# Kernel tuning notes

Hardware: AMD Instinct MI355X
Metric: run time of the kernel (lower is better)

The kernel has to match this reference:

```python
import jax, jax.numpy as jnp
import numpy as np

S = (256, 256, 256)          # MRI volume shape
N = 50000                    # number of Gaussians
T = 16                       # fixed tile edge; covers max bbox width = 2*3*sigma_max*(S-1)+2 <= 15
SIG_MIN, SIG_MAX = 0.004, 0.008  # NN-distance-based sigma range (k_sigma=1)


def setup_inputs() -> dict:
    key = jax.random.key(0)
    k1, k2, k3 = jax.random.split(key, 3)
    centers = jax.random.uniform(k1, (N, 3), dtype=jnp.float32)
    sigmas = jax.random.uniform(k2, (N,), dtype=jnp.float32, minval=SIG_MIN, maxval=SIG_MAX)
    intensities = jax.random.uniform(k3, (N,), dtype=jnp.float32)
    return {"centers": centers, "sigmas": sigmas, "intensities": intensities}


def _splat(centers, sigmas, intensities):
    dt = centers.dtype
    scale = jnp.asarray([s - 1 for s in S], dtype=dt)            # (3,) == scale_factors
    shape_f = jnp.asarray(S, dtype=dt)                           # (3,)
    shape_i = jnp.asarray(S, dtype=jnp.int32)                    # (3,)

    center_vox = centers * scale                                 # (N,3) voxel-space centers
    cutoff = 3.0 * sigmas[:, None] * scale                       # (N,3)
    # original: min_idx = max(c-cut, 0).int(); max_idx = (min(c+cut, scale)+1).int(), clipped to S
    min_idx = jnp.floor(jnp.maximum(center_vox - cutoff, 0.0)).astype(jnp.int32)          # (N,3)
    max_idx = jnp.minimum(jnp.floor(jnp.minimum(center_vox + cutoff, scale)) + 1.0,
                          shape_f).astype(jnp.int32)             # (N,3), exclusive

    ar = jnp.arange(T, dtype=jnp.int32)
    idx = min_idx[:, :, None] + ar[None, None, :]                # (N,3,T) absolute voxel idx
    valid = idx < max_idx[:, :, None]                            # (N,3,T) inside variable bbox
    idx_c = jnp.minimum(idx, shape_i[None, :, None] - 1)         # clamp for safe gather/scatter

    # grid coordinate along axis a at voxel i is i/(S_a-1) (linspace(0,1,S_a))
    coord = idx_c.astype(dt) / scale[None, :, None]              # (N,3,T)
    d = coord - centers[:, :, None]                              # (N,3,T)
    d2 = (d[:, 0, :, None, None] ** 2
          + d[:, 1, None, :, None] ** 2
          + d[:, 2, None, None, :] ** 2)                         # (N,T,T,T)
    mask = (valid[:, 0, :, None, None]
            & valid[:, 1, None, :, None]
            & valid[:, 2, None, None, :])                        # (N,T,T,T)

    inv_two_sig2 = 0.5 / (sigmas * sigmas)                       # (N,)
    contrib = intensities[:, None, None, None] * jnp.exp(-d2 * inv_two_sig2[:, None, None, None])
    contrib = jnp.where(mask, contrib, jnp.zeros((), dt))        # (N,T,T,T)

    lin = (idx_c[:, 0, :, None, None] * (S[1] * S[2])
           + idx_c[:, 1, None, :, None] * S[2]
           + idx_c[:, 2, None, None, :])                         # (N,T,T,T) flat voxel index

    vol = jnp.zeros(S[0] * S[1] * S[2], dtype=dt)
    vol = vol.at[lin.reshape(-1)].add(contrib.reshape(-1))
    return vol.reshape(S)


def reference(centers, sigmas, intensities):
    return _splat(centers, sigmas, intensities)
```

## Files before the change

### kernel.cpp

```cpp
#include <hip/hip_runtime.h>


#define NTILE 32768
#define CAP   48
#define LOG2E 1.4426950408889634f

typedef unsigned long long ull;

struct __align__(16) Pair {
    unsigned mlo, mhi;
    float cy, cz, w2;
    float ex[8];
    unsigned pad[3];
};

__global__ __launch_bounds__(256) void bin_prep_kernel(
    const float* __restrict__ centers,
    const float* __restrict__ sigmas,
    const float* __restrict__ intens,
    int*  __restrict__ counts,
    Pair* __restrict__ list,
    int N)
{
    int g = blockIdx.x * 256 + threadIdx.x;
    if (g >= N) return;
    int txi = blockIdx.y % 3;
    int tyi = blockIdx.y / 3;

    float cx = centers[3*g+0] * 255.0f;
    float cy = centers[3*g+1] * 255.0f;
    float cz = centers[3*g+2] * 255.0f;
    float sig = sigmas[g];
    float cut = 3.0f * sig * 255.0f;
    float cc[3] = {cx, cy, cz};
    int mn[3], mx[3];
    #pragma unroll
    for (int a = 0; a < 3; ++a) {
        mn[a] = (int)floorf(fmaxf(cc[a] - cut, 0.0f));
        mx[a] = (int)fminf(floorf(fminf(cc[a] + cut, 255.0f)) + 1.0f, 256.0f);
    }
    float s255 = sig * 255.0f;
    float w2 = -0.5f * LOG2E / (s255 * s255);
    float inten = intens[g];

    int t0x = mn[0] >> 3, t1x = (mx[0] - 1) >> 3;
    int t0y = mn[1] >> 3, t1y = (mx[1] - 1) >> 3;
    int t0z = mn[2] >> 3, t1z = (mx[2] - 1) >> 3;

    int tx = t0x + txi; if (tx > t1x) return;
    int ty = t0y + tyi; if (ty > t1y) return;

    int ox = tx << 3;
    int lox = max(mn[0] - ox, 0), hix = min(mx[0] - ox, 8);
    float ex[8];
    #pragma unroll
    for (int i = 0; i < 8; ++i) {
        float d = (float)(ox + i) - cx;
        float v = exp2f(d * d * w2) * inten;
        ex[i] = (i >= lox && i < hix) ? v : 0.0f;
    }

    int oy = ty << 3;
    int loy = max(mn[1] - oy, 0), hiy = min(mx[1] - oy, 8);
    ull ym = ((~0ull) << (loy << 3)) & ((~0ull) >> (64 - (hiy << 3)));

    for (int tz = t0z; tz <= t1z; ++tz) {
        int oz = tz << 3;
        int loz = max(mn[2] - oz, 0), hiz = min(mx[2] - oz, 8);
        unsigned zpat = (0xFFu >> (8 - hiz)) & (0xFFu << loz);
        ull m = (zpat * 0x0101010101010101ull) & ym;
        int t = (tx << 10) | (ty << 5) | tz;
        int slot = atomicAdd(&counts[t], 1);
        if (slot < CAP) {
            int4* q = (int4*)&list[t * CAP + slot];
            q[0] = make_int4((int)(unsigned)m, (int)(unsigned)(m >> 32),
                             __float_as_int(cy), __float_as_int(cz));
            q[1] = make_int4(__float_as_int(w2), __float_as_int(ex[0]),
                             __float_as_int(ex[1]), __float_as_int(ex[2]));
            q[2] = make_int4(__float_as_int(ex[3]), __float_as_int(ex[4]),
                             __float_as_int(ex[5]), __float_as_int(ex[6]));
            q[3] = make_int4(__float_as_int(ex[7]), 0, 0, 0);
        }
    }
}

__global__ __launch_bounds__(256) void splat_main(
    const int*  __restrict__ counts,
    const Pair* __restrict__ list,
    float* __restrict__ vol)
{
    int wid = threadIdx.x >> 6;
    int t   = __builtin_amdgcn_readfirstlane(blockIdx.x * 4 + wid);
    int ox = (t >> 10) << 3, oy = ((t >> 5) & 31) << 3, oz = (t & 31) << 3;
    int lane = threadIdx.x & 63;
    int ly = lane >> 3, lz = lane & 7;

    int n = counts[t]; if (n > CAP) n = CAP;
    const Pair* base = list + t * CAP;

    float fy = (float)(oy + ly);
    float fz = (float)(oz + lz);

    float acc[8];
    #pragma unroll
    for (int i = 0; i < 8; ++i) acc[i] = 0.0f;

    auto body = [&](const Pair& p) {
        float dy = fy - p.cy, dz = fz - p.cz;
        float e  = exp2f(fmaf(dy, dy, dz * dz) * p.w2);
        ull m = ((ull)p.mhi << 32) | (ull)p.mlo;
        float em;
        asm("v_cndmask_b32 %0, 0, %1, %2" : "=v"(em) : "v"(e), "s"(m));
        #pragma unroll
        for (int i = 0; i < 8; ++i)
            acc[i] = fmaf(p.ex[i], em, acc[i]);
    };

    Pair p0 = base[0], p1 = base[1], p2 = base[2];
    int k = 0;
    for (; k + 3 <= n; k += 3) {
        Pair a = base[k + 3];
        Pair b = base[k + 4];
        Pair c = base[k + 5];
        body(p0); body(p1); body(p2);
        p0 = a; p1 = b; p2 = c;
    }
    if (k     < n) body(p0);
    if (k + 1 < n) body(p1);
    if (k + 2 < n) body(p2);

    int ybase = ((oy + ly) << 8) + (oz + lz);
    #pragma unroll
    for (int i = 0; i < 8; ++i)
        vol[((ox + i) << 16) + ybase] = acc[i];
}

extern "C" void kernel_launch(void* const* d_in, const int* in_sizes, int n_in,
                              void* d_out, int out_size, void* d_ws, size_t ws_size,
                              hipStream_t stream) {
    const float* centers = (const float*)d_in[0];
    const float* sigmas  = (const float*)d_in[1];
    const float* intens  = (const float*)d_in[2];
    float* vol = (float*)d_out;
    const int N = in_sizes[1];

    char* ws = (char*)d_ws;
    int*  counts = (int*)ws;
    Pair* list   = (Pair*)(ws + (size_t)NTILE * sizeof(int));

    hipMemsetAsync(counts, 0, NTILE * sizeof(int), stream);

    int gblocks = (N + 255) / 256;
    bin_prep_kernel<<<dim3(gblocks, 9), 256, 0, stream>>>(centers, sigmas, intens,
                                                          counts, list, N);
    splat_main<<<NTILE / 4, 256, 0, stream>>>(counts, list, vol);
}
```

Measured before the change: 136.4 us.

## Bin each Gaussian once per z-column and gather neighbor tiles via LDS

The binning kernel now writes one compact 32-byte record per Gaussian into the tile holding its center z, instead of one 64-byte record per overlapped z tile. The x-axis Gaussian factors are rebuilt in the splat kernel by a multiplicative recurrence (q, r, s) rather than stored as eight precomputed values. Each wave stages the records of its own tile and the two z-neighbor tiles into shared memory and skips those with no z overlap. This aims to cut atomics and global traffic in the bin step and load bandwidth in the splat step. In exchange it adds per-record mask decoding, recurrence rounding error, a smaller per-tile capacity that could drop Gaussians, and the assumption that a Gaussian spans at most the adjacent z tiles.

```diff
diff --git a/kernel.cpp b/kernel.cpp
--- a/kernel.cpp
+++ b/kernel.cpp
@@ -2,16 +2,16 @@
 
 
 #define NTILE 32768
-#define CAP   48
+#define CAP   32
 #define LOG2E 1.4426950408889634f
 
 typedef unsigned long long ull;
 
-struct __align__(16) Pair {
-    unsigned mlo, mhi;
+struct __align__(16) Rec {
     float cy, cz, w2;
-    float ex[8];
-    unsigned pad[3];
+    unsigned meta;
+    float q, r, s;
+    unsigned pad;
 };
 
 __global__ __launch_bounds__(256) void bin_prep_kernel(
@@ -19,7 +19,7 @@
     const float* __restrict__ sigmas,
     const float* __restrict__ intens,
     int*  __restrict__ counts,
-    Pair* __restrict__ list,
+    Rec*  __restrict__ list,
     int N)
 {
     int g = blockIdx.x * 256 + threadIdx.x;
@@ -45,58 +45,65 @@
 
     int t0x = mn[0] >> 3, t1x = (mx[0] - 1) >> 3;
     int t0y = mn[1] >> 3, t1y = (mx[1] - 1) >> 3;
-    int t0z = mn[2] >> 3, t1z = (mx[2] - 1) >> 3;
 
     int tx = t0x + txi; if (tx > t1x) return;
     int ty = t0y + tyi; if (ty > t1y) return;
 
-    int ox = tx << 3;
+    int ox = tx << 3, oy = ty << 3;
     int lox = max(mn[0] - ox, 0), hix = min(mx[0] - ox, 8);
-    float ex[8];
-    #pragma unroll
-    for (int i = 0; i < 8; ++i) {
-        float d = (float)(ox + i) - cx;
-        float v = exp2f(d * d * w2) * inten;
-        ex[i] = (i >= lox && i < hix) ? v : 0.0f;
-    }
+    int loy = max(mn[1] - oy, 0), hiy = min(mx[1] - oy, 8);
+    unsigned xm = (0xFFu << lox) & (0xFFu >> (8 - hix));
 
-    int oy = ty << 3;
-    int loy = max(mn[1] - oy, 0), hiy = min(mx[1] - oy, 8);
-    ull ym = ((~0ull) << (loy << 3)) & ((~0ull) >> (64 - (hiy << 3)));
+    float dx0 = (float)ox - cx;
+    float q = exp2f(dx0 * dx0 * w2) * inten;
+    float r = exp2f((2.0f * dx0 + 1.0f) * w2);
+    float s = exp2f(2.0f * w2);
 
-    for (int tz = t0z; tz <= t1z; ++tz) {
-        int oz = tz << 3;
-        int loz = max(mn[2] - oz, 0), hiz = min(mx[2] - oz, 8);
-        unsigned zpat = (0xFFu >> (8 - hiz)) & (0xFFu << loz);
-        ull m = (zpat * 0x0101010101010101ull) & ym;
-        int t = (tx << 10) | (ty << 5) | tz;
-        int slot = atomicAdd(&counts[t], 1);
-        if (slot < CAP) {
-            int4* q = (int4*)&list[t * CAP + slot];
-            q[0] = make_int4((int)(unsigned)m, (int)(unsigned)(m >> 32),
-                             __float_as_int(cy), __float_as_int(cz));
-            q[1] = make_int4(__float_as_int(w2), __float_as_int(ex[0]),
-                             __float_as_int(ex[1]), __float_as_int(ex[2]));
-            q[2] = make_int4(__float_as_int(ex[3]), __float_as_int(ex[4]),
-                             __float_as_int(ex[5]), __float_as_int(ex[6]));
-            q[3] = make_int4(__float_as_int(ex[7]), 0, 0, 0);
-        }
+    int tzc = ((int)cz) >> 3;
+    int t = (tx << 10) | (ty << 5) | tzc;
+    unsigned meta = xm | ((unsigned)mn[2] << 8) | ((unsigned)(mx[2] - 1) << 16)
+                  | ((unsigned)loy << 24) | ((unsigned)hiy << 27);
+
+    int slot = atomicAdd(&counts[t], 1);
+    if (slot < CAP) {
+        int4* p = (int4*)&list[(size_t)t * CAP + slot];
+        p[0] = make_int4(__float_as_int(cy), __float_as_int(cz),
+                         __float_as_int(w2), (int)meta);
+        p[1] = make_int4(__float_as_int(q), __float_as_int(r),
+                         __float_as_int(s), 0);
     }
 }
 
 __global__ __launch_bounds__(256) void splat_main(
     const int*  __restrict__ counts,
-    const Pair* __restrict__ list,
+    const Rec*  __restrict__ list,
     float* __restrict__ vol)
 {
+    __shared__ int4 sh[4][(3 * CAP + 2) * 2];
+
     int wid = threadIdx.x >> 6;
-    int t   = __builtin_amdgcn_readfirstlane(blockIdx.x * 4 + wid);
+    int lane = threadIdx.x & 63;
+    int t = __builtin_amdgcn_readfirstlane(blockIdx.x * 4 + wid);
     int ox = (t >> 10) << 3, oy = ((t >> 5) & 31) << 3, oz = (t & 31) << 3;
-    int lane = threadIdx.x & 63;
+    int tz = t & 31;
     int ly = lane >> 3, lz = lane & 7;
 
-    int n = counts[t]; if (n > CAP) n = CAP;
-    const Pair* base = list + t * CAP;
+    int c0 = (tz > 0)  ? counts[t - 1] : 0;  if (c0 > CAP) c0 = CAP;
+    int c1 = counts[t];                       if (c1 > CAP) c1 = CAP;
+    int c2 = (tz < 31) ? counts[t + 1] : 0;  if (c2 > CAP) c2 = CAP;
+    int n01 = c0 + c1, ntot = n01 + c2;
+
+    const int4* s0 = (const int4*)(list + (long)(t - 1) * CAP);
+    const int4* s1 = (const int4*)(list + (long)t * CAP);
+    const int4* s2 = (const int4*)(list + (long)(t + 1) * CAP);
+
+    for (int k = lane; k < 2 * ntot; k += 64) {
+        const int4* src; int off;
+        if (k < 2 * c0)       { src = s0; off = k; }
+        else if (k < 2 * n01) { src = s1; off = k - 2 * c0; }
+        else                  { src = s2; off = k - 2 * n01; }
+        sh[wid][k] = src[off];
+    }
 
     float fy = (float)(oy + ly);
     float fz = (float)(oz + lz);
@@ -105,29 +112,47 @@
     #pragma unroll
     for (int i = 0; i < 8; ++i) acc[i] = 0.0f;
 
-    auto body = [&](const Pair& p) {
-        float dy = fy - p.cy, dz = fz - p.cz;
-        float e  = exp2f(fmaf(dy, dy, dz * dz) * p.w2);
-        ull m = ((ull)p.mhi << 32) | (ull)p.mlo;
-        float em;
-        asm("v_cndmask_b32 %0, 0, %1, %2" : "=v"(em) : "v"(e), "s"(m));
-        #pragma unroll
-        for (int i = 0; i < 8; ++i)
-            acc[i] = fmaf(p.ex[i], em, acc[i]);
-    };
+    const int4* P = sh[wid];
 
-    Pair p0 = base[0], p1 = base[1], p2 = base[2];
-    int k = 0;
-    for (; k + 3 <= n; k += 3) {
-        Pair a = base[k + 3];
-        Pair b = base[k + 4];
-        Pair c = base[k + 5];
-        body(p0); body(p1); body(p2);
-        p0 = a; p1 = b; p2 = c;
+    int4 a0 = P[0], a1 = P[1];
+    for (int k = 0; k < ntot; ++k) {
+        int b = (k + 1) << 1;
+        int4 b0 = P[b], b1 = P[b + 1];
+
+        unsigned meta = (unsigned)__builtin_amdgcn_readfirstlane(a0.w);
+        int mnz  = (int)((meta >> 8)  & 0xFF);
+        int mxzi = (int)((meta >> 16) & 0xFF);
+        int loz = mnz - oz;      if (loz < 0) loz = 0;
+        int hiz = mxzi + 1 - oz; if (hiz > 8) hiz = 8;
+        if (loz < hiz) {
+            unsigned xm  = meta & 0xFF;
+            int loy_ = (int)((meta >> 24) & 7);
+            int hiy_ = (int)((meta >> 27) & 0xF);
+            ull ym = ((~0ull) << (loy_ << 3)) & ((~0ull) >> (64 - (hiy_ << 3)));
+            unsigned zpat = (0xFFu >> (8 - hiz)) & (0xFFu << loz);
+            unsigned zrep = zpat * 0x01010101u;
+            ull m = (((ull)zrep << 32) | (ull)zrep) & ym;
+
+            float cyv = __int_as_float(a0.x), czv = __int_as_float(a0.y);
+            float w2v = __int_as_float(a0.z);
+            float qv = __int_as_float(a1.x), rv = __int_as_float(a1.y);
+            float sv = __int_as_float(a1.z);
+
+            float dy = fy - cyv, dz = fz - czv;
+            float e = exp2f(fmaf(dy, dy, dz * dz) * w2v);
+            float em;
+            asm("v_cndmask_b32 %0, 0, %1, %2" : "=v"(em) : "v"(e), "s"(m));
+
+            float ei = qv, ri = rv;
+            #pragma unroll
+            for (int i = 0; i < 8; ++i) {
+                float v = (xm & (1u << i)) ? ei : 0.0f;
+                acc[i] = fmaf(v, em, acc[i]);
+                ei *= ri; ri *= sv;
+            }
+        }
+        a0 = b0; a1 = b1;
     }
-    if (k     < n) body(p0);
-    if (k + 1 < n) body(p1);
-    if (k + 2 < n) body(p2);
 
     int ybase = ((oy + ly) << 8) + (oz + lz);
     #pragma unroll
@@ -146,9 +171,9 @@
 
     char* ws = (char*)d_ws;
     int*  counts = (int*)ws;
-    Pair* list   = (Pair*)(ws + (size_t)NTILE * sizeof(int));
+    Rec*  list   = (Rec*)(ws + (size_t)NTILE * sizeof(int));
 
-    hipMemsetAsync(counts, 0, NTILE * sizeof(int), stream);
+    hipMemsetAsync(counts, 0, (size_t)NTILE * sizeof(int), stream);
 
     int gblocks = (N + 255) / 256;
     bin_prep_kernel<<<dim3(gblocks, 9), 256, 0, stream>>>(centers, sigmas, intens,
```

Measured after the change: 139.3 us. 1.02x slower.
